# Optimization experiments

Hardware: AMD Instinct MI355X
Metric: run time of the kernel (lower is better)

## Reference

```python
import jax, jax.numpy as jnp
import numpy as np

N_NODES = 1_000_000   # rows in the feature table
N_TARGETS = 100_000   # target nodes being aggregated
NUM_SAMPLES = 32      # neighbors sampled per node (with replacement)
D = 128               # in_channels == out_channels for mean aggregation


def setup_inputs() -> dict:
    key = jax.random.key(0)
    k1, k2 = jax.random.split(key)
    features = jax.random.normal(k1, (N_NODES, D), dtype=jnp.float32)
    # Pre-sampled neighbor indices (replaces per-node np.random.choice loop;
    # sampling with replacement yields a fixed-width [n, num_samples] matrix).
    neighbor_idx = jax.random.randint(k2, (N_TARGETS, NUM_SAMPLES), 0, N_NODES, dtype=jnp.int64)
    return {"features": features, "neighbor_idx": neighbor_idx}


def reference(features, neighbor_idx):
    # Fused gather + segment mean: out[i] = mean_j features[neighbor_idx[i, j]]
    gathered = jnp.take(features, neighbor_idx, axis=0)   # [n, num_samples, D]
    return jnp.mean(gathered, axis=1)                     # [n, D]
```

## Files before the change

### kernel.cpp

```cpp
#include <hip/hip_runtime.h>


constexpr int D = 128;
constexpr int S = 32;
constexpr int D4 = D / 4;
constexpr int N_WAVES = 8192;

__global__ __launch_bounds__(256) void Aggregator_20710332301461_kernel(
    const float* __restrict__ feat,
    const int* __restrict__ idx,
    float* __restrict__ out,
    int n_targets)
{
    const int lane = threadIdx.x & 63;
    const int half = lane >> 5;
    const int sub = lane & 31;
    const int w = blockIdx.x * (blockDim.x >> 6) + (threadIdx.x >> 6);

    const float4* __restrict__ f4 = reinterpret_cast<const float4*>(feat);
    float4* __restrict__ o4 = reinterpret_cast<float4*>(out);

    const int n_pairs = (n_targets + 1) >> 1;

    for (int p = w; p < n_pairs; p += N_WAVES) {
        const int t = 2 * p + half;
        const bool valid = (t < n_targets);

        int myidx = 0;
        if (valid) myidx = idx[t * S + sub];

        float4 acc = {0.f, 0.f, 0.f, 0.f};
        #pragma unroll
        for (int j = 0; j < S; ++j) {
            const int r = __shfl(myidx, half * 32 + j);
            const float4 v = f4[(size_t)r * D4 + sub];
            acc.x += v.x;
            acc.y += v.y;
            acc.z += v.z;
            acc.w += v.w;
        }

        if (valid) {
            float4 res;
            res.x = acc.x * (1.f / S);
            res.y = acc.y * (1.f / S);
            res.z = acc.z * (1.f / S);
            res.w = acc.w * (1.f / S);
            o4[(size_t)t * D4 + sub] = res;
        }
    }
}

extern "C" void kernel_launch(void* const* d_in, const int* in_sizes, int n_in,
                              void* d_out, int out_size, void* d_ws, size_t ws_size,
                              hipStream_t stream) {
    const float* feat = (const float*)d_in[0];
    const int* idx = (const int*)d_in[1];
    float* out = (float*)d_out;

    const int n_targets = out_size / D;

    const int block = 256;
    const int grid = N_WAVES / (block / 64);

    Aggregator_20710332301461_kernel<<<grid, block, 0, stream>>>(feat, idx, out, n_targets);
}
```

Baseline: 239.0 us.

## Split gather into four index-range phases to localize feature-table reads

Runs the kernel four times. Each pass gathers only neighbors whose row index lies in one quarter of the feature table (index >> 18), compacting the matching indices through shared memory with a ballot. Partial sums accumulate in the output buffer and the last pass applies the mean. The aim is to keep each pass's working set (about 128 MB of features) resident in the last-level cache and cut random HBM traffic. In exchange it adds three extra read-modify-write passes over the output, reloads the index array every pass, and pays for extra launches. The loop is also data-dependent with divergent trip counts.

```diff
diff --git a/kernel.cpp b/kernel.cpp
--- a/kernel.cpp
+++ b/kernel.cpp
@@ -5,22 +5,28 @@
 constexpr int S = 32;
 constexpr int D4 = D / 4;
 constexpr int N_WAVES = 8192;
+constexpr int NPHASE = 4;
+constexpr int PH_SHIFT = 18;
 
 __global__ __launch_bounds__(256) void Aggregator_20710332301461_kernel(
     const float* __restrict__ feat,
     const int* __restrict__ idx,
     float* __restrict__ out,
-    int n_targets)
+    int n_targets, int ph)
 {
+    __shared__ int comp[4][2][32];
+
     const int lane = threadIdx.x & 63;
     const int half = lane >> 5;
     const int sub = lane & 31;
-    const int w = blockIdx.x * (blockDim.x >> 6) + (threadIdx.x >> 6);
+    const int wib = threadIdx.x >> 6;
+    const int w = blockIdx.x * 4 + wib;
 
     const float4* __restrict__ f4 = reinterpret_cast<const float4*>(feat);
     float4* __restrict__ o4 = reinterpret_cast<float4*>(out);
 
     const int n_pairs = (n_targets + 1) >> 1;
+    const bool last = (ph == NPHASE - 1);
 
     for (int p = w; p < n_pairs; p += N_WAVES) {
         const int t = 2 * p + half;
@@ -29,24 +35,52 @@
         int myidx = 0;
         if (valid) myidx = idx[t * S + sub];
 
+        if (sub == 0) comp[wib][half][0] = 0;
+
+        const bool inw = valid && ((myidx >> PH_SHIFT) == ph);
+        const unsigned long long bal = __ballot(inw);
+        const unsigned mask_h = (unsigned)(bal >> (half ? 32 : 0));
+        if (inw) {
+            const int pos = __popc(mask_h & ((1u << sub) - 1u));
+            comp[wib][half][pos] = myidx;
+        }
+        const int c0 = __popc((unsigned)(bal & 0xFFFFFFFFull));
+        const int c1 = __popc((unsigned)(bal >> 32));
+        const int cme = half ? c1 : c0;
+        const int cmax = (c0 > c1) ? c0 : c1;
+
         float4 acc = {0.f, 0.f, 0.f, 0.f};
-        #pragma unroll
-        for (int j = 0; j < S; ++j) {
-            const int r = __shfl(myidx, half * 32 + j);
+        #pragma unroll 4
+        for (int j = 0; j < cmax; ++j) {
+            const int jj = (j < cme) ? j : 0;
+            const int r = comp[wib][half][jj];
             const float4 v = f4[(size_t)r * D4 + sub];
-            acc.x += v.x;
-            acc.y += v.y;
-            acc.z += v.z;
-            acc.w += v.w;
+            if (j < cme) {
+                acc.x += v.x;
+                acc.y += v.y;
+                acc.z += v.z;
+                acc.w += v.w;
+            }
         }
 
         if (valid) {
-            float4 res;
-            res.x = acc.x * (1.f / S);
-            res.y = acc.y * (1.f / S);
-            res.z = acc.z * (1.f / S);
-            res.w = acc.w * (1.f / S);
-            o4[(size_t)t * D4 + sub] = res;
+            const size_t o = (size_t)t * D4 + sub;
+            if (ph == 0) {
+                o4[o] = acc;
+            } else if (!last) {
+                float4 prev = o4[o];
+                prev.x += acc.x; prev.y += acc.y;
+                prev.z += acc.z; prev.w += acc.w;
+                o4[o] = prev;
+            } else {
+                float4 prev = o4[o];
+                float4 res;
+                res.x = (prev.x + acc.x) * (1.f / S);
+                res.y = (prev.y + acc.y) * (1.f / S);
+                res.z = (prev.z + acc.z) * (1.f / S);
+                res.w = (prev.w + acc.w) * (1.f / S);
+                o4[o] = res;
+            }
         }
     }
 }
@@ -63,5 +97,8 @@
     const int block = 256;
     const int grid = N_WAVES / (block / 64);
 
-    Aggregator_20710332301461_kernel<<<grid, block, 0, stream>>>(feat, idx, out, n_targets);
+    for (int ph = 0; ph < NPHASE; ++ph) {
+        Aggregator_20710332301461_kernel<<<grid, block, 0, stream>>>(
+            feat, idx, out, n_targets, ph);
+    }
 }
```

New measurement: 306.8 us. +28.4%, slower.
